# Performance work log

Measured on AMD Instinct MI355X. Metric: run time of the kernel, lower is better.

The kernel has to match this reference:

```python
import jax, jax.numpy as jnp
import numpy as np

K = 128   # per-head dim == input dim
H = 8     # heads
B = 2
T = 2048


def setup_inputs() -> dict:
    key = jax.random.key(0)
    ks = jax.random.split(key, 6)
    s_in = 1.0 / np.sqrt(K)
    s_out = 1.0 / np.sqrt(K * H)
    return {
        "x": jax.random.normal(ks[0], (B, T, K), dtype=jnp.float32),
        # Linear weights stored as (in, out); torch Linear init ~ U(-1/sqrt(in), 1/sqrt(in))
        "Wq": jax.random.uniform(ks[1], (K, K * H), jnp.float32, -s_in, s_in),
        "Wk": jax.random.uniform(ks[2], (K, K * H), jnp.float32, -s_in, s_in),
        "Wv": jax.random.uniform(ks[3], (K, K * H), jnp.float32, -s_in, s_in),
        "Wo": jax.random.uniform(ks[4], (K * H, K), jnp.float32, -s_out, s_out),
        "bo": jax.random.uniform(ks[5], (K,), jnp.float32, -s_out, s_out),
    }


def reference(x, Wq, Wk, Wv, Wo, bo):
    b, t, k = x.shape
    h = H
    scale = k ** 0.25
    # projections -> [b, t, h, k]
    q = (x @ Wq).reshape(b, t, h, k) / scale
    ke = (x @ Wk).reshape(b, t, h, k) / scale
    v = (x @ Wv).reshape(b, t, h, k)
    # scores: [b, h, t, t]
    scores = jnp.einsum('bihk,bjhk->bhij', q, ke)
    # causal mask: positions j > i get -inf (diagonal kept)
    causal = jnp.tril(jnp.ones((t, t), dtype=bool))
    scores = jnp.where(causal[None, None], scores, -jnp.inf)
    p = jax.nn.softmax(scores, axis=-1)
    out = jnp.einsum('bhij,bjhk->bihk', p, v).reshape(b, t, h * k)
    return out @ Wo + bo
```

## Files before the change

### kernel.cpp

```cpp
#include <hip/hip_runtime.h>

typedef __bf16 bf16;
typedef __bf16 bf16x4 __attribute__((ext_vector_type(4)));
typedef __bf16 bf16x8 __attribute__((ext_vector_type(8)));
typedef float f32x4 __attribute__((ext_vector_type(4)));
typedef float f32x16 __attribute__((ext_vector_type(16)));
typedef int i32x4 __attribute__((ext_vector_type(4)));

#define MFMA16(a, b, c) __builtin_amdgcn_mfma_f32_16x16x32_bf16((a), (b), (c), 0, 0, 0)
#define MFMA32(a, b, c) __builtin_amdgcn_mfma_f32_32x32x16_bf16((a), (b), (c), 0, 0, 0)

__device__ __forceinline__ int swz16(int r, int c) { return (c ^ (r & 15)); }
__device__ __forceinline__ int swz8(int r, int c) { return (c ^ (r & 7)); }

__device__ __forceinline__ int cvt_pk_bf16(float lo, float hi) {
  int r;
  asm("v_cvt_pk_bf16_f32 %0, %1, %2" : "=v"(r) : "v"(lo), "v"(hi));
  return r;
}

__global__ __launch_bounds__(256) void trW_kernel(
    const float* __restrict__ Wq, const float* __restrict__ Wk,
    const float* __restrict__ Wv, const float* __restrict__ Wo,
    bf16* __restrict__ outbase) {
  __shared__ bf16 tile[32][33];
  const int z = blockIdx.z;
  const float* ib = (z == 0) ? Wq : (z == 1) ? Wk : (z == 2) ? Wv : Wo;
  bf16* ob = outbase + (size_t)z * 131072;
  const int R = (z < 3) ? 128 : 1024;
  const int C = (z < 3) ? 1024 : 128;
  int r0 = (z < 3) ? blockIdx.y * 32 : blockIdx.x * 32;
  int c0 = (z < 3) ? blockIdx.x * 32 : blockIdx.y * 32;
  int tx = threadIdx.x & 31, ty = threadIdx.x >> 5;
#pragma unroll
  for (int i = 0; i < 4; ++i) {
    int r = ty + i * 8;
    tile[r][tx] = (bf16)ib[(size_t)(r0 + r) * C + (c0 + tx)];
  }
  __syncthreads();
#pragma unroll
  for (int i = 0; i < 4; ++i) {
    int r = ty + i * 8;
    ob[(size_t)(c0 + r) * R + (r0 + tx)] = tile[tx][r];
  }
}

__global__ __launch_bounds__(256) void proj_gemm(
    const float* __restrict__ x, const bf16* __restrict__ Wqt,
    const bf16* __restrict__ Wkt, const bf16* __restrict__ Wvt,
    bf16* __restrict__ Qb, bf16* __restrict__ Kb, bf16* __restrict__ Vt) {
  __shared__ __align__(16) bf16 As[128 * 128];
  __shared__ __align__(16) bf16 Bs[128 * 128];
  const int mt = blockIdx.x;
  const int nt = blockIdx.y;
  const int matid = nt >> 3, h = nt & 7;
  const bf16* W = (matid == 0) ? Wqt : (matid == 1) ? Wkt : Wvt;
  const int tid = threadIdx.x;
  const bf16* sb = W + (size_t)h * 128 * 128;
#pragma unroll
  for (int i = 0; i < 8; ++i) {
    int c = tid + i * 256;
    int r = c >> 4, cc = c & 15;
    const f32x4* p = (const f32x4*)(x + (size_t)(mt * 128 + r) * 128 + cc * 8);
    f32x4 a = p[0], b = p[1];
    bf16x8 o;
#pragma unroll
    for (int j = 0; j < 4; ++j) { o[j] = (bf16)a[j]; o[4 + j] = (bf16)b[j]; }
    *(bf16x8*)&As[r * 128 + swz16(r, cc) * 8] = o;
  }
#pragma unroll
  for (int i = 0; i < 8; ++i) {
    int c = tid + i * 256;
    int r = c >> 4, cc = c & 15;
    *(bf16x8*)&Bs[r * 128 + swz16(r, cc) * 8] = *(const bf16x8*)(sb + (size_t)r * 128 + cc * 8);
  }
  __syncthreads();
  const int wave = tid >> 6, lane = tid & 63;
  const int wr = (wave >> 1) * 64, wc = (wave & 1) * 64;
  const int lr = lane & 15, lkb = lane >> 4;
  const f32x4 FZ = {0.f, 0.f, 0.f, 0.f};
  f32x4 acc[4][4];
#pragma unroll
  for (int mf = 0; mf < 4; ++mf)
#pragma unroll
    for (int nf = 0; nf < 4; ++nf) acc[mf][nf] = FZ;
  const bool qk = (matid < 2);
#pragma unroll
  for (int ks = 0; ks < 4; ++ks) {
    bf16x8 a[4], b[4];
#pragma unroll
    for (int mf = 0; mf < 4; ++mf) {
      int r = wr + mf * 16 + lr;
      a[mf] = *(const bf16x8*)&As[r * 128 + swz16(r, ks * 4 + lkb) * 8];
    }
#pragma unroll
    for (int nf = 0; nf < 4; ++nf) {
      int r = wc + nf * 16 + lr;
      b[nf] = *(const bf16x8*)&Bs[r * 128 + swz16(r, ks * 4 + lkb) * 8];
    }
    if (qk) {
#pragma unroll
      for (int mf = 0; mf < 4; ++mf)
#pragma unroll
        for (int nf = 0; nf < 4; ++nf) acc[mf][nf] = MFMA16(b[nf], a[mf], acc[mf][nf]);
    } else {
#pragma unroll
      for (int mf = 0; mf < 4; ++mf)
#pragma unroll
        for (int nf = 0; nf < 4; ++nf) acc[mf][nf] = MFMA16(a[mf], b[nf], acc[mf][nf]);
    }
  }
  const int rb = lkb * 4;
  if (qk) {
    bf16* Out = (matid == 0) ? Qb : Kb;
#pragma unroll
    for (int mf = 0; mf < 4; ++mf)
#pragma unroll
      for (int nf = 0; nf < 4; ++nf) {
        int m = mt * 128 + wr + mf * 16 + lr;
        int d0 = wc + nf * 16 + rb;
        int bb = m >> 11, t = m & 2047;
        bf16x4 vv;
#pragma unroll
        for (int r = 0; r < 4; ++r) vv[r] = (bf16)acc[mf][nf][r];
        *(bf16x4*)(Out + ((size_t)(bb * 8 + h) * 2048 + t) * 128 + d0) = vv;
      }
  } else {
#pragma unroll
    for (int mf = 0; mf < 4; ++mf)
#pragma unroll
      for (int nf = 0; nf < 4; ++nf) {
        int d = wc + nf * 16 + lr;
        int m0 = mt * 128 + wr + mf * 16 + rb;
        int bb = m0 >> 11, t0 = m0 & 2047;
        bf16x4 vv;
#pragma unroll
        for (int r = 0; r < 4; ++r) vv[r] = (bf16)acc[mf][nf][r];
        *(bf16x4*)(Vt + ((size_t)(bb * 8 + h) * 128 + d) * 2048 + t0) = vv;
      }
  }
}

__global__ __launch_bounds__(256) void attn_kernel(
    bf16* __restrict__ Qb, const bf16* __restrict__ Kb, const bf16* __restrict__ Vt) {
  extern __shared__ char smem[];
  const int bid = blockIdx.x;
  const int qt = 31 - (bid >> 4);
  const int bh = bid & 15;
  const int nT = qt + 1;
  const int h0 = (nT + 1) >> 1, h1 = nT - h0;
  const bf16* Qh = Qb + (size_t)bh * 2048 * 128;
  bf16* Qw = Qb + (size_t)bh * 2048 * 128;
  const bf16* Kh = Kb + (size_t)bh * 2048 * 128;
  const bf16* Vh = Vt + (size_t)bh * 128 * 2048;
  const int tid = threadIdx.x, lane = tid & 63;
  const int g = tid >> 7;
  const int tg = tid & 127;
  const int wig = (tid >> 6) & 1;
  const int lq = lane & 31;
  const int hi = lane >> 5;
  const int q0w = qt * 64 + wig * 32;
  const int hg = g ? h1 : h0;
  const int tbase = g ? h0 : 0;
  const float SCL = 0.12751744f;

  bf16* Ks = (bf16*)(smem + g * 32768);
  bf16* Vs = (bf16*)(smem + g * 32768 + 16384);

  const int krow = tg >> 4, kcc = tg & 15;
  const int kchb = kcc ^ krow;
  const bf16* ksrc0 = Kh + (size_t)krow * 128 + kcc * 8;
  const int vrow = tg >> 3, vcc = tg & 7;
  bf16* vdst0 = Vs + vrow * 64 + (vcc ^ (vrow & 7)) * 8;
  const bf16* vsrc0 = Vh + (size_t)vrow * 2048 + vcc * 8;

  bf16x8 qf[8];
#pragma unroll
  for (int ks = 0; ks < 8; ++ks)
    qf[ks] = *(const bf16x8*)(Qh + (size_t)(q0w + lq) * 128 + ks * 16 + hi * 8);

  float mrun = -__builtin_inff(), lrun = 0.f;
  f32x16 O[4];
#pragma unroll
  for (int dt = 0; dt < 4; ++dt)
#pragma unroll
    for (int r = 0; r < 16; ++r) O[dt][r] = 0.f;

  bf16x8 kpre[8], vpre[8];
  if (hg > 0) {
    const size_t ko = (size_t)tbase * 8192, vo = (size_t)tbase * 64;
#pragma unroll
    for (int i = 0; i < 8; ++i) kpre[i] = *(const bf16x8*)(ksrc0 + ko + i * 1024);
#pragma unroll
    for (int i = 0; i < 8; ++i) vpre[i] = *(const bf16x8*)(vsrc0 + vo + i * 32768);
  }

  for (int it = 0; it < h0; ++it) {
    const bool act = (it < hg);
    const int kvt = tbase + it;
    const int kv0 = kvt * 64;
    __syncthreads();
    if (act) {
#pragma unroll
      for (int i = 0; i < 8; ++i)
        *(bf16x8*)(Ks + (krow + 8 * i) * 128 + (kchb ^ ((i & 1) << 3)) * 8) = kpre[i];
#pragma unroll
      for (int i = 0; i < 8; ++i) *(bf16x8*)(vdst0 + i * 1024) = vpre[i];
    }
    __syncthreads();
    if (it + 1 < hg) {
      const size_t ko = (size_t)(kvt + 1) * 8192, vo = (size_t)(kvt + 1) * 64;
#pragma unroll
      for (int i = 0; i < 8; ++i) kpre[i] = *(const bf16x8*)(ksrc0 + ko + i * 1024);
#pragma unroll
      for (int i = 0; i < 8; ++i) vpre[i] = *(const bf16x8*)(vsrc0 + vo + i * 32768);
    }
    if (!act) continue;

    f32x16 p0, p1;
#pragma unroll
    for (int r = 0; r < 16; ++r) { p0[r] = 0.f; p1[r] = 0.f; }
#pragma unroll
    for (int ks = 0; ks < 8; ++ks) {
      int c = (ks * 2 + hi);
      bf16x8 ka = *(const bf16x8*)&Ks[lq * 128 + (c ^ (lq & 15)) * 8];
      bf16x8 kb = *(const bf16x8*)&Ks[(32 + lq) * 128 + (c ^ (lq & 15)) * 8];
      p0 = MFMA32(ka, qf[ks], p0);
      p1 = MFMA32(kb, qf[ks], p1);
    }
    if (kvt == qt) {
      const int qg = q0w + lq;
#pragma unroll
      for (int r = 0; r < 16; ++r) {
        int kvr = kv0 + (r & 3) + 8 * (r >> 2) + 4 * hi;
        if (kvr > qg) p0[r] = -__builtin_inff();
        if (kvr + 32 > qg) p1[r] = -__builtin_inff();
      }
    }
    float pm = -__builtin_inff();
#pragma unroll
    for (int r = 0; r < 16; ++r) pm = fmaxf(pm, fmaxf(p0[r], p1[r]));
    pm = fmaxf(pm, __shfl_xor(pm, 32, 64));
    float mnew = fmaxf(mrun, pm * SCL);
    float alpha = exp2f(mrun - mnew);
    mrun = mnew;
    float ps = 0.f;
#pragma unroll
    for (int r = 0; r < 16; ++r) {
      float a = exp2f(__builtin_fmaf(p0[r], SCL, -mnew));
      float b = exp2f(__builtin_fmaf(p1[r], SCL, -mnew));
      p0[r] = a; p1[r] = b;
      ps += a + b;
    }
    ps += __shfl_xor(ps, 32, 64);
    lrun = lrun * alpha + ps;
#pragma unroll
    for (int dt = 0; dt < 4; ++dt)
#pragma unroll
      for (int r = 0; r < 16; ++r) O[dt][r] *= alpha;

    int w[16];
#pragma unroll
    for (int i = 0; i < 8; ++i) w[i] = cvt_pk_bf16(p0[2 * i], p0[2 * i + 1]);
#pragma unroll
    for (int i = 0; i < 8; ++i) w[8 + i] = cvt_pk_bf16(p1[2 * i], p1[2 * i + 1]);
    bf16x8 pa[4];
#pragma unroll
    for (int t4 = 0; t4 < 4; ++t4) {
      int b0 = t4 * 4;
      int e0 = __shfl_xor(w[b0 + 0], 32, 64);
      int e1 = __shfl_xor(w[b0 + 1], 32, 64);
      int e2 = __shfl_xor(w[b0 + 2], 32, 64);
      int e3 = __shfl_xor(w[b0 + 3], 32, 64);
      i32x4 f;
      f[0] = hi ? e2 : w[b0 + 0];
      f[1] = hi ? e3 : w[b0 + 1];
      f[2] = hi ? w[b0 + 2] : e0;
      f[3] = hi ? w[b0 + 3] : e1;
      pa[t4] = __builtin_bit_cast(bf16x8, f);
    }
#pragma unroll
    for (int dt = 0; dt < 4; ++dt) {
      int rr = dt * 32 + lq;
#pragma unroll
      for (int ks2 = 0; ks2 < 4; ++ks2) {
        bf16x8 va = *(const bf16x8*)&Vs[rr * 64 + ((ks2 * 2 + hi) ^ (rr & 7)) * 8];
        O[dt] = MFMA32(va, pa[ks2], O[dt]);
      }
    }
  }

  float* Om = (float*)smem;
  float* Lm = (float*)(smem + 32768);
  float* Ll = (float*)(smem + 32768 + 256);
  const int qq = wig * 32 + lq;
  __syncthreads();
  if (g == 1) {
#pragma unroll
    for (int dt = 0; dt < 4; ++dt)
#pragma unroll
      for (int r = 0; r < 16; ++r)
        Om[(dt * 32 + (r & 3) + 8 * (r >> 2) + 4 * hi) * 64 + qq] = O[dt][r];
    if (!hi) { Lm[qq] = mrun; Ll[qq] = lrun; }
  }
  __syncthreads();
  if (g == 0) {
    float m1 = Lm[qq], l1 = Ll[qq];
    float mf = fmaxf(mrun, m1);
    float a0 = exp2f(mrun - mf), a1 = exp2f(m1 - mf);
    float inv = 1.f / (lrun * a0 + l1 * a1);
    bf16* qwrow = Qw + (size_t)(q0w + lq) * 128;
#pragma unroll
    for (int dt = 0; dt < 4; ++dt) {
#pragma unroll
      for (int rq = 0; rq < 4; ++rq) {
        bf16x4 vv;
#pragma unroll
        for (int j = 0; j < 4; ++j) {
          int r = rq * 4 + j;
          float o1 = Om[(dt * 32 + j + 8 * rq + 4 * hi) * 64 + qq];
          vv[j] = (bf16)((O[dt][r] * a0 + o1 * a1) * inv);
        }
        *(bf16x4*)(qwrow + dt * 32 + 8 * rq + 4 * hi) = vv;
      }
    }
  }
}

__global__ __launch_bounds__(256) void outproj_kernel(
    const bf16* __restrict__ AO, const bf16* __restrict__ Wot,
    const float* __restrict__ bo, float* __restrict__ out) {
  __shared__ __align__(16) bf16 As[16 * 128];
  __shared__ __align__(16) bf16 Bs[128 * 128];
  const f32x4 FZ = {0.f, 0.f, 0.f, 0.f};
  const int mt = blockIdx.x;
  const int tid = threadIdx.x, wave = tid >> 6, lane = tid & 63;
  const int lr = lane & 15, lkb = lane >> 4, rb = lkb * 4;
  const int wc = wave * 32;
  f32x4 acc[2];
  acc[0] = FZ; acc[1] = FZ;
  for (int kt = 0; kt < 8; ++kt) {
    __syncthreads();
    {
      int r = tid >> 4, cc = tid & 15;
      int m = mt * 16 + r, bb = m >> 11, t = m & 2047;
      *(bf16x8*)&As[r * 128 + swz16(r, cc) * 8] =
          *(const bf16x8*)(AO + ((size_t)(bb * 8 + kt) * 2048 + t) * 128 + cc * 8);
    }
#pragma unroll
    for (int i = 0; i < 8; ++i) {
      int c = tid + i * 256;
      int r = c >> 4, cc = c & 15;
      *(bf16x8*)&Bs[r * 128 + swz16(r, cc) * 8] =
          *(const bf16x8*)(Wot + (size_t)r * 1024 + kt * 128 + cc * 8);
    }
    __syncthreads();
#pragma unroll
    for (int ks = 0; ks < 4; ++ks) {
      bf16x8 a = *(const bf16x8*)&As[lr * 128 + swz16(lr, ks * 4 + lkb) * 8];
#pragma unroll
      for (int nf = 0; nf < 2; ++nf) {
        int r = wc + nf * 16 + lr;
        bf16x8 b = *(const bf16x8*)&Bs[r * 128 + swz16(r, ks * 4 + lkb) * 8];
        acc[nf] = MFMA16(a, b, acc[nf]);
      }
    }
  }
#pragma unroll
  for (int nf = 0; nf < 2; ++nf)
#pragma unroll
    for (int r = 0; r < 4; ++r) {
      int m = mt * 16 + rb + r;
      int n = wc + nf * 16 + lr;
      out[(size_t)m * 128 + n] = acc[nf][r] + bo[n];
    }
}

extern "C" void kernel_launch(void* const* d_in, const int* in_sizes, int n_in,
                              void* d_out, int out_size, void* d_ws, size_t ws_size,
                              hipStream_t stream) {
  (void)in_sizes; (void)n_in; (void)out_size; (void)ws_size;
  const float* x  = (const float*)d_in[0];
  const float* Wq = (const float*)d_in[1];
  const float* Wk = (const float*)d_in[2];
  const float* Wv = (const float*)d_in[3];
  const float* Wo = (const float*)d_in[4];
  const float* bo = (const float*)d_in[5];
  float* out = (float*)d_out;

  bf16* ws  = (bf16*)d_ws;
  bf16* Wqt = ws;
  bf16* Wkt = Wqt + 131072;
  bf16* Wvt = Wkt + 131072;
  bf16* Wot = Wvt + 131072;
  bf16* Qb  = Wot + 131072;
  bf16* Kb  = Qb + 4194304;
  bf16* Vt  = Kb + 4194304;

  trW_kernel<<<dim3(32, 4, 4), 256, 0, stream>>>(Wq, Wk, Wv, Wo, Wqt);
  proj_gemm<<<dim3(32, 24, 1), 256, 0, stream>>>(x, Wqt, Wkt, Wvt, Qb, Kb, Vt);
  attn_kernel<<<dim3(512, 1, 1), 256, 65536, stream>>>(Qb, Kb, Vt);
  outproj_kernel<<<dim3(256, 1, 1), 256, 0, stream>>>(Qb, Wot, bo, out);
}
```

Before: 148.7 us.

## Store Q/K/V in MFMA-fragment order and load attention operands directly from global

The projection GEMM now writes Q, K and V in a layout pre-tiled to match the MFMA 32x32 operand fragments. The attention kernel can then read K and V straight from global/L2 into registers, with no LDS staging or barriers. Attention is split into 1024 blocks of 128 threads, each owning a 32-query tile, with a balanced query-tile ordering across blocks. The online softmax also skips the rescale of O and l unless the running max grows by more than a threshold. The risks are more redundant global traffic, since each wave reloads K/V with no sharing, and lost register prefetch overlap.

```diff
diff --git a/kernel.cpp b/kernel.cpp
--- a/kernel.cpp
+++ b/kernel.cpp
@@ -11,7 +11,6 @@
 #define MFMA32(a, b, c) __builtin_amdgcn_mfma_f32_32x32x16_bf16((a), (b), (c), 0, 0, 0)
 
 __device__ __forceinline__ int swz16(int r, int c) { return (c ^ (r & 15)); }
-__device__ __forceinline__ int swz8(int r, int c) { return (c ^ (r & 7)); }
 
 __device__ __forceinline__ int cvt_pk_bf16(float lo, float hi) {
   int r;
@@ -48,7 +47,7 @@
 __global__ __launch_bounds__(256) void proj_gemm(
     const float* __restrict__ x, const bf16* __restrict__ Wqt,
     const bf16* __restrict__ Wkt, const bf16* __restrict__ Wvt,
-    bf16* __restrict__ Qb, bf16* __restrict__ Kb, bf16* __restrict__ Vt) {
+    bf16* __restrict__ Qf, bf16* __restrict__ Kf, bf16* __restrict__ Vf) {
   __shared__ __align__(16) bf16 As[128 * 128];
   __shared__ __align__(16) bf16 Bs[128 * 128];
   const int mt = blockIdx.x;
@@ -112,7 +111,7 @@
   }
   const int rb = lkb * 4;
   if (qk) {
-    bf16* Out = (matid == 0) ? Qb : Kb;
+    bf16* Out = (matid == 0) ? Qf : Kf;
 #pragma unroll
     for (int mf = 0; mf < 4; ++mf)
 #pragma unroll
@@ -123,7 +122,10 @@
         bf16x4 vv;
 #pragma unroll
         for (int r = 0; r < 4; ++r) vv[r] = (bf16)acc[mf][nf][r];
-        *(bf16x4*)(Out + ((size_t)(bb * 8 + h) * 2048 + t) * 128 + d0) = vv;
+        size_t e = (size_t)(bb * 8 + h) * 262144
+                 + (size_t)(((t >> 5) * 8 + (d0 >> 4)) * 512 + ((d0 >> 3) & 1) * 256
+                            + (t & 31) * 8 + (d0 & 7));
+        *(bf16x4*)(Out + e) = vv;
       }
   } else {
 #pragma unroll
@@ -136,48 +138,42 @@
         bf16x4 vv;
 #pragma unroll
         for (int r = 0; r < 4; ++r) vv[r] = (bf16)acc[mf][nf][r];
-        *(bf16x4*)(Vt + ((size_t)(bb * 8 + h) * 128 + d) * 2048 + t0) = vv;
-      }
-  }
-}
-
-__global__ __launch_bounds__(256) void attn_kernel(
-    bf16* __restrict__ Qb, const bf16* __restrict__ Kb, const bf16* __restrict__ Vt) {
-  extern __shared__ char smem[];
+        size_t e = (size_t)(bb * 8 + h) * 262144
+                 + (size_t)((d >> 5) * 65536 + (t0 >> 4) * 512 + ((t0 >> 3) & 1) * 256
+                            + (d & 31) * 8 + (t0 & 7));
+        *(bf16x4*)(Vf + e) = vv;
+      }
+  }
+}
+
+__global__ __launch_bounds__(128) void attn_kernel(
+    bf16* __restrict__ Qf, const bf16* __restrict__ Kf, const bf16* __restrict__ Vf) {
+  __shared__ float Om[128 * 32];
+  __shared__ float Lm[32];
+  __shared__ float Ll[32];
   const int bid = blockIdx.x;
-  const int qt = 31 - (bid >> 4);
-  const int bh = bid & 15;
-  const int nT = qt + 1;
+  const int bh = (bid & 7) | (((bid >> 3) & 1) << 3);
+  const int j = bid >> 4;
+  const int v = j & 15, m4 = j >> 4;
+  const int qt = (m4 == 0) ? v : (m4 == 1) ? 31 - v : (m4 == 2) ? 32 + v : 63 - v;
+  const int nT = (qt >> 1) + 1;
   const int h0 = (nT + 1) >> 1, h1 = nT - h0;
-  const bf16* Qh = Qb + (size_t)bh * 2048 * 128;
-  bf16* Qw = Qb + (size_t)bh * 2048 * 128;
-  const bf16* Kh = Kb + (size_t)bh * 2048 * 128;
-  const bf16* Vh = Vt + (size_t)bh * 128 * 2048;
-  const int tid = threadIdx.x, lane = tid & 63;
-  const int g = tid >> 7;
-  const int tg = tid & 127;
-  const int wig = (tid >> 6) & 1;
-  const int lq = lane & 31;
-  const int hi = lane >> 5;
-  const int q0w = qt * 64 + wig * 32;
+  const int tid = threadIdx.x;
+  const int g = tid >> 6, lane = tid & 63;
+  const int lq = lane & 31, hi = lane >> 5;
+  const int q0 = qt * 32;
   const int hg = g ? h1 : h0;
-  const int tbase = g ? h0 : 0;
+  const int tb = g ? h0 : 0;
+  const bf16* Qh = Qf + (size_t)bh * 262144;
+  const bf16* Kh = Kf + (size_t)bh * 262144;
+  const bf16* Vh = Vf + (size_t)bh * 262144;
   const float SCL = 0.12751744f;
-
-  bf16* Ks = (bf16*)(smem + g * 32768);
-  bf16* Vs = (bf16*)(smem + g * 32768 + 16384);
-
-  const int krow = tg >> 4, kcc = tg & 15;
-  const int kchb = kcc ^ krow;
-  const bf16* ksrc0 = Kh + (size_t)krow * 128 + kcc * 8;
-  const int vrow = tg >> 3, vcc = tg & 7;
-  bf16* vdst0 = Vs + vrow * 64 + (vcc ^ (vrow & 7)) * 8;
-  const bf16* vsrc0 = Vh + (size_t)vrow * 2048 + vcc * 8;
+  const int lo = hi * 256 + lq * 8;
 
   bf16x8 qf[8];
 #pragma unroll
   for (int ks = 0; ks < 8; ++ks)
-    qf[ks] = *(const bf16x8*)(Qh + (size_t)(q0w + lq) * 128 + ks * 16 + hi * 8);
+    qf[ks] = *(const bf16x8*)(Qh + qt * 4096 + ks * 512 + lo);
 
   float mrun = -__builtin_inff(), lrun = 0.f;
   f32x16 O[4];
@@ -186,50 +182,24 @@
 #pragma unroll
     for (int r = 0; r < 16; ++r) O[dt][r] = 0.f;
 
-  bf16x8 kpre[8], vpre[8];
-  if (hg > 0) {
-    const size_t ko = (size_t)tbase * 8192, vo = (size_t)tbase * 64;
-#pragma unroll
-    for (int i = 0; i < 8; ++i) kpre[i] = *(const bf16x8*)(ksrc0 + ko + i * 1024);
-#pragma unroll
-    for (int i = 0; i < 8; ++i) vpre[i] = *(const bf16x8*)(vsrc0 + vo + i * 32768);
-  }
-
-  for (int it = 0; it < h0; ++it) {
-    const bool act = (it < hg);
-    const int kvt = tbase + it;
+  for (int it = 0; it < hg; ++it) {
+    const int kvt = tb + it;
     const int kv0 = kvt * 64;
-    __syncthreads();
-    if (act) {
-#pragma unroll
-      for (int i = 0; i < 8; ++i)
-        *(bf16x8*)(Ks + (krow + 8 * i) * 128 + (kchb ^ ((i & 1) << 3)) * 8) = kpre[i];
-#pragma unroll
-      for (int i = 0; i < 8; ++i) *(bf16x8*)(vdst0 + i * 1024) = vpre[i];
-    }
-    __syncthreads();
-    if (it + 1 < hg) {
-      const size_t ko = (size_t)(kvt + 1) * 8192, vo = (size_t)(kvt + 1) * 64;
-#pragma unroll
-      for (int i = 0; i < 8; ++i) kpre[i] = *(const bf16x8*)(ksrc0 + ko + i * 1024);
-#pragma unroll
-      for (int i = 0; i < 8; ++i) vpre[i] = *(const bf16x8*)(vsrc0 + vo + i * 32768);
-    }
-    if (!act) continue;
-
+    const bf16* kbase = Kh + kvt * 8192 + lo;
+    bf16x8 ka[8], kb[8];
+#pragma unroll
+    for (int i = 0; i < 8; ++i) ka[i] = *(const bf16x8*)(kbase + i * 512);
+#pragma unroll
+    for (int i = 0; i < 8; ++i) kb[i] = *(const bf16x8*)(kbase + 4096 + i * 512);
     f32x16 p0, p1;
 #pragma unroll
     for (int r = 0; r < 16; ++r) { p0[r] = 0.f; p1[r] = 0.f; }
 #pragma unroll
-    for (int ks = 0; ks < 8; ++ks) {
-      int c = (ks * 2 + hi);
-      bf16x8 ka = *(const bf16x8*)&Ks[lq * 128 + (c ^ (lq & 15)) * 8];
-      bf16x8 kb = *(const bf16x8*)&Ks[(32 + lq) * 128 + (c ^ (lq & 15)) * 8];
-      p0 = MFMA32(ka, qf[ks], p0);
-      p1 = MFMA32(kb, qf[ks], p1);
-    }
-    if (kvt == qt) {
-      const int qg = q0w + lq;
+    for (int ks = 0; ks < 8; ++ks) p0 = MFMA32(ka[ks], qf[ks], p0);
+#pragma unroll
+    for (int ks = 0; ks < 8; ++ks) p1 = MFMA32(kb[ks], qf[ks], p1);
+    if (kvt == (qt >> 1)) {
+      const int qg = q0 + lq;
 #pragma unroll
       for (int r = 0; r < 16; ++r) {
         int kvr = kv0 + (r & 3) + 8 * (r >> 2) + 4 * hi;
@@ -241,24 +211,27 @@
 #pragma unroll
     for (int r = 0; r < 16; ++r) pm = fmaxf(pm, fmaxf(p0[r], p1[r]));
     pm = fmaxf(pm, __shfl_xor(pm, 32, 64));
-    float mnew = fmaxf(mrun, pm * SCL);
-    float alpha = exp2f(mrun - mnew);
-    mrun = mnew;
+    float pmS = pm * SCL;
+    if (!__all(pmS <= mrun + 8.f)) {
+      float mnew = fmaxf(mrun, pmS);
+      float alpha = exp2f(mrun - mnew);
+      mrun = mnew;
+      lrun *= alpha;
+#pragma unroll
+      for (int dt = 0; dt < 4; ++dt)
+#pragma unroll
+        for (int r = 0; r < 16; ++r) O[dt][r] *= alpha;
+    }
     float ps = 0.f;
 #pragma unroll
     for (int r = 0; r < 16; ++r) {
-      float a = exp2f(__builtin_fmaf(p0[r], SCL, -mnew));
-      float b = exp2f(__builtin_fmaf(p1[r], SCL, -mnew));
+      float a = exp2f(__builtin_fmaf(p0[r], SCL, -mrun));
+      float b = exp2f(__builtin_fmaf(p1[r], SCL, -mrun));
       p0[r] = a; p1[r] = b;
       ps += a + b;
     }
     ps += __shfl_xor(ps, 32, 64);
-    lrun = lrun * alpha + ps;
-#pragma unroll
-    for (int dt = 0; dt < 4; ++dt)
-#pragma unroll
-      for (int r = 0; r < 16; ++r) O[dt][r] *= alpha;
-
+    lrun += ps;
     int w[16];
 #pragma unroll
     for (int i = 0; i < 8; ++i) w[i] = cvt_pk_bf16(p0[2 * i], p0[2 * i + 1]);
@@ -279,49 +252,48 @@
       f[3] = hi ? w[b0 + 3] : e1;
       pa[t4] = __builtin_bit_cast(bf16x8, f);
     }
+    const bf16* vbase = Vh + (kvt * 4) * 512 + lo;
 #pragma unroll
     for (int dt = 0; dt < 4; ++dt) {
-      int rr = dt * 32 + lq;
-#pragma unroll
-      for (int ks2 = 0; ks2 < 4; ++ks2) {
-        bf16x8 va = *(const bf16x8*)&Vs[rr * 64 + ((ks2 * 2 + hi) ^ (rr & 7)) * 8];
-        O[dt] = MFMA32(va, pa[ks2], O[dt]);
-      }
-    }
-  }
-
-  float* Om = (float*)smem;
-  float* Lm = (float*)(smem + 32768);
-  float* Ll = (float*)(smem + 32768 + 256);
-  const int qq = wig * 32 + lq;
-  __syncthreads();
+      bf16x8 va0 = *(const bf16x8*)(vbase + dt * 65536 + 0 * 512);
+      bf16x8 va1 = *(const bf16x8*)(vbase + dt * 65536 + 1 * 512);
+      bf16x8 va2 = *(const bf16x8*)(vbase + dt * 65536 + 2 * 512);
+      bf16x8 va3 = *(const bf16x8*)(vbase + dt * 65536 + 3 * 512);
+      O[dt] = MFMA32(va0, pa[0], O[dt]);
+      O[dt] = MFMA32(va1, pa[1], O[dt]);
+      O[dt] = MFMA32(va2, pa[2], O[dt]);
+      O[dt] = MFMA32(va3, pa[3], O[dt]);
+    }
+  }
+
   if (g == 1) {
 #pragma unroll
     for (int dt = 0; dt < 4; ++dt)
 #pragma unroll
       for (int r = 0; r < 16; ++r)
-        Om[(dt * 32 + (r & 3) + 8 * (r >> 2) + 4 * hi) * 64 + qq] = O[dt][r];
-    if (!hi) { Lm[qq] = mrun; Ll[qq] = lrun; }
+        Om[(dt * 32 + (r & 3) + 8 * (r >> 2) + 4 * hi) * 32 + lq] = O[dt][r];
+    if (!hi) { Lm[lq] = mrun; Ll[lq] = lrun; }
   }
   __syncthreads();
   if (g == 0) {
-    float m1 = Lm[qq], l1 = Ll[qq];
-    float mf = fmaxf(mrun, m1);
-    float a0 = exp2f(mrun - mf), a1 = exp2f(m1 - mf);
+    float m1 = Lm[lq], l1 = Ll[lq];
+    float mF = fmaxf(mrun, m1);
+    float a0 = exp2f(mrun - mF), a1 = exp2f(m1 - mF);
     float inv = 1.f / (lrun * a0 + l1 * a1);
-    bf16* qwrow = Qw + (size_t)(q0w + lq) * 128;
+    bf16* qw = Qf + (size_t)bh * 262144 + qt * 4096 + lq * 8 + 4 * hi;
 #pragma unroll
     for (int dt = 0; dt < 4; ++dt) {
 #pragma unroll
       for (int rq = 0; rq < 4; ++rq) {
         bf16x4 vv;
 #pragma unroll
-        for (int j = 0; j < 4; ++j) {
-          int r = rq * 4 + j;
-          float o1 = Om[(dt * 32 + j + 8 * rq + 4 * hi) * 64 + qq];
-          vv[j] = (bf16)((O[dt][r] * a0 + o1 * a1) * inv);
+        for (int jj = 0; jj < 4; ++jj) {
+          int r = rq * 4 + jj;
+          int d = dt * 32 + jj + 8 * rq + 4 * hi;
+          float o1 = Om[d * 32 + lq];
+          vv[jj] = (bf16)((O[dt][r] * a0 + o1 * a1) * inv);
         }
-        *(bf16x4*)(qwrow + dt * 32 + 8 * rq + 4 * hi) = vv;
+        *(bf16x4*)(qw + (dt * 2 + (rq >> 1)) * 512 + (rq & 1) * 256) = vv;
       }
     }
   }
@@ -344,8 +316,9 @@
     {
       int r = tid >> 4, cc = tid & 15;
       int m = mt * 16 + r, bb = m >> 11, t = m & 2047;
-      *(bf16x8*)&As[r * 128 + swz16(r, cc) * 8] =
-          *(const bf16x8*)(AO + ((size_t)(bb * 8 + kt) * 2048 + t) * 128 + cc * 8);
+      const bf16* src = AO + (size_t)(bb * 8 + kt) * 262144
+          + ((t >> 5) * 8 + (cc >> 1)) * 512 + (cc & 1) * 256 + (t & 31) * 8;
+      *(bf16x8*)&As[r * 128 + swz16(r, cc) * 8] = *(const bf16x8*)src;
     }
 #pragma unroll
     for (int i = 0; i < 8; ++i) {
@@ -393,12 +366,12 @@
   bf16* Wkt = Wqt + 131072;
   bf16* Wvt = Wkt + 131072;
   bf16* Wot = Wvt + 131072;
-  bf16* Qb  = Wot + 131072;
-  bf16* Kb  = Qb + 4194304;
-  bf16* Vt  = Kb + 4194304;
+  bf16* Qf  = Wot + 131072;
+  bf16* Kf  = Qf + 4194304;
+  bf16* Vf  = Kf + 4194304;
 
   trW_kernel<<<dim3(32, 4, 4), 256, 0, stream>>>(Wq, Wk, Wv, Wo, Wqt);
-  proj_gemm<<<dim3(32, 24, 1), 256, 0, stream>>>(x, Wqt, Wkt, Wvt, Qb, Kb, Vt);
-  attn_kernel<<<dim3(512, 1, 1), 256, 65536, stream>>>(Qb, Kb, Vt);
-  outproj_kernel<<<dim3(256, 1, 1), 256, 0, stream>>>(Qb, Wot, bo, out);
-}
+  proj_gemm<<<dim3(32, 24, 1), 256, 0, stream>>>(x, Wqt, Wkt, Wvt, Qf, Kf, Vf);
+  attn_kernel<<<dim3(1024, 1, 1), 128, 0, stream>>>(Qf, Kf, Vf);
+  outproj_kernel<<<dim3(256, 1, 1), 256, 0, stream>>>(Qf, Wot, bo, out);
+}
```

After: 146.5 us. Within noise of the previous version (-1.5%).
